# Kernel tuning notes

Hardware: AMD Instinct MI355X
Metric: run time of the kernel (lower is better)

The kernel has to match this reference:

```python
import jax, jax.numpy as jnp
import numpy as np

# module config (init_kwargs)
AH, AW = 14, 14            # aligned_height, aligned_width
SCALE = 0.25               # spatial_scale
RATIO = 2                  # sampling_ratio
SHIFT = 0.0                # spatial_shift (added in feature-map coords)
HALF_PART = 0              # 0 = full box
ROI_SCALE = 1.0            # box rescale about its center


def setup_inputs() -> dict:
    key = jax.random.key(0)
    kf, kb, kx, ky, kw, kh = jax.random.split(key, 6)
    B, C, H, W = 2, 256, 200, 272
    N = 256
    features = jax.random.normal(kf, (B, C, H, W), dtype=jnp.float32)
    img_h, img_w = H / SCALE, W / SCALE
    bidx = jax.random.randint(kb, (N,), 0, B).astype(jnp.float32)
    x1 = jax.random.uniform(kx, (N,)) * (img_w * 0.6)
    y1 = jax.random.uniform(ky, (N,)) * (img_h * 0.6)
    bw = 32.0 + jax.random.uniform(kw, (N,)) * (img_w * 0.35)
    bh = 32.0 + jax.random.uniform(kh, (N,)) * (img_h * 0.35)
    rois = jnp.stack([bidx, x1, y1, x1 + bw, y1 + bh], axis=1).astype(jnp.float32)
    return {"features": features, "rois": rois}


def _lin_idx(coord, size):
    # bilinear index/weight prep with RoIAlign boundary rules
    valid = (coord > -1.0) & (coord < float(size))
    c = jnp.clip(coord, 0.0, float(size - 1))
    lo = jnp.floor(c)
    hi = jnp.minimum(lo + 1.0, float(size - 1))
    frac = c - lo
    return lo.astype(jnp.int32), hi.astype(jnp.int32), frac, valid.astype(coord.dtype)


def _roi_mask_align(features, rois):
    B, C, H, W = features.shape
    N = rois.shape[0]
    PH, PW, r = AH + 1, AW + 1, RATIO
    b = rois[:, 0].astype(jnp.int32)
    # to feature-map coords, with roi_scale about the box center and spatial_shift
    x1, y1, x2, y2 = (rois[:, 1] * SCALE, rois[:, 2] * SCALE,
                      rois[:, 3] * SCALE, rois[:, 4] * SCALE)
    cx, cy = 0.5 * (x1 + x2), 0.5 * (y1 + y2)
    hw, hh = 0.5 * (x2 - x1) * ROI_SCALE, 0.5 * (y2 - y1) * ROI_SCALE
    x1, x2 = cx - hw + SHIFT, cx + hw + SHIFT
    y1, y2 = cy - hh + SHIFT, cy + hh + SHIFT
    roi_w = jnp.maximum(x2 - x1, 1.0)
    roi_h = jnp.maximum(y2 - y1, 1.0)
    bin_w = roi_w / PW
    bin_h = roi_h / PH
    # sample coords, separable: sx [N, PW*r], sy [N, PH*r]
    ix = jnp.arange(PW * r, dtype=jnp.float32)
    iy = jnp.arange(PH * r, dtype=jnp.float32)
    sx = x1[:, None] + (ix[None, :] + 0.5) * (bin_w[:, None] / r)
    sy = y1[:, None] + (iy[None, :] + 0.5) * (bin_h[:, None] / r)
    y_lo, y_hi, fy, vy = _lin_idx(sy, H)
    x_lo, x_hi, fx, vx = _lin_idx(sx, W)
    featsT = jnp.transpose(features, (0, 2, 3, 1))  # [B,H,W,C]
    bb = b[:, None, None]
    gather = lambda yi, xi: featsT[bb, yi[:, :, None], xi[:, None, :]]  # [N,Sy,Sx,C]
    wy0, wy1 = 1.0 - fy, fy
    wx0, wx1 = 1.0 - fx, fx
    val = (gather(y_lo, x_lo) * (wy0[:, :, None] * wx0[:, None, :])[..., None]
           + gather(y_lo, x_hi) * (wy0[:, :, None] * wx1[:, None, :])[..., None]
           + gather(y_hi, x_lo) * (wy1[:, :, None] * wx0[:, None, :])[..., None]
           + gather(y_hi, x_hi) * (wy1[:, :, None] * wx1[:, None, :])[..., None])
    val = val * (vy[:, :, None] * vx[:, None, :])[..., None]
    # average the r*r samples per bin -> [N, PH, PW, C]
    val = val.reshape(N, PH, r, PW, r, C).mean(axis=(2, 4))
    return jnp.transpose(val, (0, 3, 1, 2))  # [N, C, PH, PW]


def reference(features, rois):
    x = _roi_mask_align(features, rois)  # [N, C, AH+1, AW+1]
    # avg_pool2d(kernel=2, stride=1)
    out = 0.25 * (x[..., :-1, :-1] + x[..., 1:, :-1]
                  + x[..., :-1, 1:] + x[..., 1:, 1:])
    return out  # [N, C, AH, AW]
```

## Files before the change

kernel.cpp:

```cpp
#include <hip/hip_runtime.h>


#define AH_  14
#define AW_  14
#define C_   256
#define H_   200
#define W_   272
#define HW_  (H_ * W_)
#define CPB  4

__global__ __launch_bounds__(128, 8)
void roi_mask_align_avg_kernel(const float* __restrict__ feat,
                               const float* __restrict__ rois,
                               float* __restrict__ out) {
    __shared__ float Ls[2][CPB * 7 * AW_];

    const int p   = blockIdx.x;
    const int xcd = p & 7;
    const int q   = p >> 3;
    const int n   = q & 255;
    const int cgi = q >> 8;
    const int cg  = cgi * 8 + xcd;
    const int c0  = cg * CPB;

    const int tid  = threadIdx.x;
    const int wave = tid >> 6;
    const int lane = tid & 63;
    const int half = lane >> 5;
    const int ix   = lane & 31;

    const float r0f = rois[n * 5 + 0];
    const float x1s = rois[n * 5 + 1] * 0.25f;
    const float y1s = rois[n * 5 + 2] * 0.25f;
    const float x2s = rois[n * 5 + 3] * 0.25f;
    const float y2s = rois[n * 5 + 4] * 0.25f;
    const int   b   = (int)r0f;

    const float cx = 0.5f * (x1s + x2s), cy = 0.5f * (y1s + y2s);
    const float hw = 0.5f * (x2s - x1s), hh = 0.5f * (y2s - y1s);
    const float x1 = cx - hw, x2 = cx + hw;
    const float y1 = cy - hh, y2 = cy + hh;
    const float roi_w = fmaxf(x2 - x1, 1.0f);
    const float roi_h = fmaxf(y2 - y1, 1.0f);
    const float sub_w = roi_w * (1.0f / 15.0f) * 0.5f;
    const float sub_h = roi_h * (1.0f / 15.0f) * 0.5f;

    const float sx  = x1 + ((float)ix + 0.5f) * sub_w;
    const bool  vx_ = (sx > -1.0f) && (sx < (float)W_) && (ix < 30);
    const float ccx = fminf(fmaxf(sx, 0.0f), (float)(W_ - 1));
    const float lox = floorf(ccx);
    const int   xl  = (int)lox;
    const int   xh  = min(xl + 1, W_ - 1);
    const float fx  = ccx - lox;
    const float vmx = vx_ ? 1.0f : 0.0f;
    const float wx0 = (1.0f - fx) * vmx;
    const float wx1 = fx * vmx;

    const float* __restrict__ bpA = feat + ((size_t)b * C_ + c0) * (size_t)HW_;
    const float* __restrict__ bpB = bpA + 2 * HW_;
    const int vx0 = half * HW_ + xl;
    const int vx1 = half * HW_ + xh;

    const int  aw   = ix >> 1;
    const bool emit = ((lane & 1) == 0) && (aw < AW_);
    float* __restrict__ Lw = Ls[wave];

    float alo0 = 0.f, alo1 = 0.f, ahi0 = 0.f, ahi1 = 0.f;
    float blo0 = 0.f, blo1 = 0.f, bhi0 = 0.f, bhi1 = 0.f;
    int   pyl = -100, pyh = -100;

    const int iy0 = wave * 14;
    float prevSA = 0.f, prevSB = 0.f;

    for (int kk = 0; kk < 8; ++kk) {
        float PA = 0.f, PB = 0.f;
        #pragma unroll
        for (int r = 0; r < 2; ++r) {
            const int iy = iy0 + 2 * kk + r;
            const float sy  = y1 + ((float)iy + 0.5f) * sub_h;
            const bool  vy_ = (sy > -1.0f) && (sy < (float)H_);
            const float ccy = fminf(fmaxf(sy, 0.0f), (float)(H_ - 1));
            const float loy = floorf(ccy);
            const float fy  = ccy - loy;
            const float vmy = vy_ ? 1.0f : 0.0f;
            const float wy0 = (1.0f - fy) * vmy;
            const float wy1 = fy * vmy;

            const int yl_s = __builtin_amdgcn_readfirstlane((int)loy);
            const int yh_s = min(yl_s + 1, H_ - 1);

            if (yl_s == pyl && yh_s == pyh) {
            } else if (yl_s == pyh) {
                alo0 = ahi0; alo1 = ahi1; blo0 = bhi0; blo1 = bhi1;
                const float* __restrict__ pa = bpA + yh_s * W_;
                const float* __restrict__ pb = bpB + yh_s * W_;
                ahi0 = pa[vx0]; ahi1 = pa[vx1];
                bhi0 = pb[vx0]; bhi1 = pb[vx1];
            } else {
                const float* __restrict__ pal = bpA + yl_s * W_;
                const float* __restrict__ pah = bpA + yh_s * W_;
                const float* __restrict__ pbl = bpB + yl_s * W_;
                const float* __restrict__ pbh = bpB + yh_s * W_;
                alo0 = pal[vx0]; alo1 = pal[vx1];
                ahi0 = pah[vx0]; ahi1 = pah[vx1];
                blo0 = pbl[vx0]; blo1 = pbl[vx1];
                bhi0 = pbh[vx0]; bhi1 = pbh[vx1];
            }
            pyl = yl_s; pyh = yh_s;

            const float w00 = wy0 * wx0, w01 = wy0 * wx1;
            const float w10 = wy1 * wx0, w11 = wy1 * wx1;
            PA += alo0 * w00 + alo1 * w01 + ahi0 * w10 + ahi1 * w11;
            PB += blo0 * w00 + blo1 * w01 + bhi0 * w10 + bhi1 * w11;
        }
        const float tA = PA + __shfl_xor(PA, 1, 64);
        const float uA = tA + __shfl_down(tA, 2, 64);
        const float tB = PB + __shfl_xor(PB, 1, 64);
        const float uB = tB + __shfl_down(tB, 2, 64);
        if (kk > 0 && emit) {
            const int row = kk - 1;
            Lw[half * 98 + row * AW_ + aw]       = (prevSA + uA) * 0.0625f;
            Lw[(2 + half) * 98 + row * AW_ + aw] = (prevSB + uB) * 0.0625f;
        }
        prevSA = uA;
        prevSB = uB;
    }

    float* __restrict__ op = out + ((size_t)n * C_ + c0) * (AH_ * AW_);
    for (int o = lane; o < CPB * 7 * AW_; o += 64) {
        const int ch  = o / 98;
        const int rem = o - ch * 98;
        op[ch * (AH_ * AW_) + wave * 98 + rem] = Lw[o];
    }
}

extern "C" void kernel_launch(void* const* d_in, const int* in_sizes, int n_in,
                              void* d_out, int out_size, void* d_ws, size_t ws_size,
                              hipStream_t stream) {
    const float* feat = (const float*)d_in[0];
    const float* rois = (const float*)d_in[1];
    float* out = (float*)d_out;
    const int grid = 256 * (C_ / CPB);
    roi_mask_align_avg_kernel<<<grid, 128, 0, stream>>>(feat, rois, out);
}
```

Baseline: 245.5 us.

## Stage feature rows into LDS via coalesced global_load_lds instead of scattered gathers

```diff
diff --git a/kernel.cpp b/kernel.cpp
--- a/kernel.cpp
+++ b/kernel.cpp
@@ -8,12 +8,18 @@
 #define W_   272
 #define HW_  (H_ * W_)
 #define CPB  4
+#define WBUF 1424
 
-__global__ __launch_bounds__(128, 8)
+#define GLOAD_LDS16(g, l)                                                     \
+  __builtin_amdgcn_global_load_lds(                                           \
+      (const __attribute__((address_space(1))) void*)(g),                     \
+      (__attribute__((address_space(3))) void*)(l), 16, 0, 0)
+
+__global__ __launch_bounds__(128)
 void roi_mask_align_avg_kernel(const float* __restrict__ feat,
                                const float* __restrict__ rois,
                                float* __restrict__ out) {
-    __shared__ float Ls[2][CPB * 7 * AW_];
+    __shared__ float Ls[2][WBUF];
 
     const int p   = blockIdx.x;
     const int xcd = p & 7;
@@ -28,6 +34,9 @@
     const int lane = tid & 63;
     const int half = lane >> 5;
     const int ix   = lane & 31;
+
+    float* __restrict__ LsW = Ls[wave];
+    if (lane == 0) LsW[1024] = 0.0f;
 
     const float r0f = rois[n * 5 + 0];
     const float x1s = rois[n * 5 + 1] * 0.25f;
@@ -56,14 +65,20 @@
     const float wx0 = (1.0f - fx) * vmx;
     const float wx1 = fx * vmx;
 
+    const int s0    = __builtin_amdgcn_readfirstlane(xl);
+    const int s0c   = min(s0, W_ - 128);
+    const int xh29  = __builtin_amdgcn_readlane(xh, 29);
+    const int spanrel = xh29 - s0c;
+    const bool ldact  = (ix * 4) <= spanrel;
+    const int iA    = half * 128 + (xl - s0c);
+
     const float* __restrict__ bpA = feat + ((size_t)b * C_ + c0) * (size_t)HW_;
-    const float* __restrict__ bpB = bpA + 2 * HW_;
-    const int vx0 = half * HW_ + xl;
-    const int vx1 = half * HW_ + xh;
+    const float* __restrict__ gA  = bpA + (size_t)half * HW_ + s0c + 4 * ix;
+    const float* __restrict__ gB  = gA + 2 * HW_;
 
     const int  aw   = ix >> 1;
     const bool emit = ((lane & 1) == 0) && (aw < AW_);
-    float* __restrict__ Lw = Ls[wave];
+    float* __restrict__ Ow = LsW + 1028;
 
     float alo0 = 0.f, alo1 = 0.f, ahi0 = 0.f, ahi1 = 0.f;
     float blo0 = 0.f, blo1 = 0.f, bhi0 = 0.f, bhi1 = 0.f;
@@ -92,19 +107,29 @@
             if (yl_s == pyl && yh_s == pyh) {
             } else if (yl_s == pyh) {
                 alo0 = ahi0; alo1 = ahi1; blo0 = bhi0; blo1 = bhi1;
-                const float* __restrict__ pa = bpA + yh_s * W_;
-                const float* __restrict__ pb = bpB + yh_s * W_;
-                ahi0 = pa[vx0]; ahi1 = pa[vx1];
-                bhi0 = pb[vx0]; bhi1 = pb[vx1];
+                const int ro = yh_s * W_;
+                asm volatile("s_waitcnt lgkmcnt(0)" ::: "memory");
+                if (ldact) {
+                    GLOAD_LDS16(gA + ro, LsW + 512);
+                    GLOAD_LDS16(gB + ro, LsW + 768);
+                }
+                asm volatile("s_waitcnt vmcnt(0)" ::: "memory");
+                ahi0 = LsW[512 + iA]; ahi1 = LsW[512 + iA + 1];
+                bhi0 = LsW[768 + iA]; bhi1 = LsW[768 + iA + 1];
             } else {
-                const float* __restrict__ pal = bpA + yl_s * W_;
-                const float* __restrict__ pah = bpA + yh_s * W_;
-                const float* __restrict__ pbl = bpB + yl_s * W_;
-                const float* __restrict__ pbh = bpB + yh_s * W_;
-                alo0 = pal[vx0]; alo1 = pal[vx1];
-                ahi0 = pah[vx0]; ahi1 = pah[vx1];
-                blo0 = pbl[vx0]; blo1 = pbl[vx1];
-                bhi0 = pbh[vx0]; bhi1 = pbh[vx1];
+                const int rlo = yl_s * W_, rhi = yh_s * W_;
+                asm volatile("s_waitcnt lgkmcnt(0)" ::: "memory");
+                if (ldact) {
+                    GLOAD_LDS16(gA + rlo, LsW + 0);
+                    GLOAD_LDS16(gB + rlo, LsW + 256);
+                    GLOAD_LDS16(gA + rhi, LsW + 512);
+                    GLOAD_LDS16(gB + rhi, LsW + 768);
+                }
+                asm volatile("s_waitcnt vmcnt(0)" ::: "memory");
+                alo0 = LsW[iA];       alo1 = LsW[iA + 1];
+                blo0 = LsW[256 + iA]; blo1 = LsW[256 + iA + 1];
+                ahi0 = LsW[512 + iA]; ahi1 = LsW[512 + iA + 1];
+                bhi0 = LsW[768 + iA]; bhi1 = LsW[768 + iA + 1];
             }
             pyl = yl_s; pyh = yh_s;
 
@@ -119,8 +144,8 @@
         const float uB = tB + __shfl_down(tB, 2, 64);
         if (kk > 0 && emit) {
             const int row = kk - 1;
-            Lw[half * 98 + row * AW_ + aw]       = (prevSA + uA) * 0.0625f;
-            Lw[(2 + half) * 98 + row * AW_ + aw] = (prevSB + uB) * 0.0625f;
+            Ow[half * 98 + row * AW_ + aw]       = (prevSA + uA) * 0.0625f;
+            Ow[(2 + half) * 98 + row * AW_ + aw] = (prevSB + uB) * 0.0625f;
         }
         prevSA = uA;
         prevSB = uB;
@@ -130,7 +155,7 @@
     for (int o = lane; o < CPB * 7 * AW_; o += 64) {
         const int ch  = o / 98;
         const int rem = o - ch * 98;
-        op[ch * (AH_ * AW_) + wave * 98 + rem] = Lw[o];
+        op[ch * (AH_ * AW_) + wave * 98 + rem] = Ow[o];
     }
 }
 
```

Result: faster. 233.5 us (-4.9%).
